# Optimization experiments

Measured on AMD Instinct MI355X. Metric: run time of the kernel, lower is better.

## Reference

```python
import jax, jax.numpy as jnp
import numpy as np

EPS = 1e-5   # torch F.layer_norm default eps
TOP_K = 20   # int(3*D^2 / (2*hr*N^2 + 10*D)) for D=768, N=196, hr=1.0
NUM_EXPERTS = 200  # 10 * TOP_K


def setup_inputs() -> dict:
    key = jax.random.key(0)
    ks = jax.random.split(key, 6)
    B, N, D = 32, 196, 768
    E, H = NUM_EXPERTS, 196  # H = int(N * hidden_ratio)
    s = 0.02
    return {
        "x": jax.random.normal(ks[0], (B, N, D), jnp.float32),
        "Wr": jax.random.normal(ks[1], (E, D), jnp.float32) * s,   # router.weight
        "W1": jax.random.normal(ks[2], (E, H, N), jnp.float32) * s,  # fc1.weight per expert
        "b1": jnp.zeros((E, H), jnp.float32),
        "W2": jax.random.normal(ks[3], (E, N, H), jnp.float32) * s,  # fc2.weight per expert
        "b2": jnp.zeros((E, N), jnp.float32),
        "Wo": jax.random.normal(ks[4], (D, D), jnp.float32) * s,     # out_proj.weight
        "bo": jnp.zeros((D,), jnp.float32),
    }


def reference(x, Wr, W1, b1, W2, b2, Wo, bo):
    B, N, D = x.shape
    E = Wr.shape[0]
    K = TOP_K

    # Router: per-sample routing on token-mean features
    logits = x.mean(axis=1) @ Wr.T                      # (B, E)
    probs = jax.nn.softmax(logits, axis=-1)             # (B, E)
    w, idx = jax.lax.top_k(probs, K)                    # (B, K) sorted desc, as torch.topk
    w = w / w.sum(axis=-1, keepdims=True)               # renormalize top-k weights

    # TokenMixer operates in (B, D, N) space: layernorm over tokens (no affine),
    # then fc1 (N->H), gelu(tanh), fc2 (H->N).
    xt = jnp.swapaxes(x, 1, 2)                          # (B, D, N)
    mu = xt.mean(axis=-1, keepdims=True)
    var = xt.var(axis=-1, keepdims=True)                # population var (matches F.layer_norm)
    z = (xt - mu) * jax.lax.rsqrt(var + EPS)            # (B, D, N)

    # Gather each sample's K expert weight matrices and batch the MLPs.
    W1g, b1g = W1[idx], b1[idx]                         # (B,K,H,N), (B,K,H)
    W2g, b2g = W2[idx], b2[idx]                         # (B,K,N,H), (B,K,N)

    h = jnp.einsum('bdn,bkhn->bkdh', z, W1g) + b1g[:, :, None, :]
    a = jax.nn.gelu(h, approximate=True)                # tanh-approx GELU
    o = jnp.einsum('bkdh,bknh->bkdn', a, W2g) + b2g[:, :, None, :]

    # Weighted combine over the K selected experts, back to (B, N, D)
    mix = jnp.einsum('bk,bkdn->bnd', w, o)

    out = mix @ Wo.T + bo                               # out_proj

    # Load-balancing aux loss (top-1 assignment fraction vs mean router prob)
    top1 = jax.nn.one_hot(idx[:, 0], E, dtype=probs.dtype)   # (B, E)
    aux = E * jnp.sum(probs.mean(axis=0) * top1.mean(axis=0))
    return out, aux
```

## Files before the change

### kernel.cpp

```cpp
#include <hip/hip_runtime.h>
#include <math.h>

constexpr int B  = 32;
constexpr int N  = 196;
constexpr int D  = 768;
constexpr int E  = 200;
constexpr int TK = 20;

constexpr int NGRP = 4;
constexpr int PRB  = 14336;
constexpr int EXB  = 114688;
constexpr int LK   = 40;

typedef __bf16 bf16x8 __attribute__((ext_vector_type(8)));
typedef __bf16 bf16x4 __attribute__((ext_vector_type(4)));
typedef float  f32x4  __attribute__((ext_vector_type(4)));
typedef long   longx2 __attribute__((ext_vector_type(2)));
typedef unsigned char uchar;

#define GLDS16(gp, lp)                                                        \
  __builtin_amdgcn_global_load_lds(                                           \
      (const __attribute__((address_space(1))) void*)(gp),                    \
      (__attribute__((address_space(3))) void*)(lp), 16, 0, 0)

#define WAITVM12  __builtin_amdgcn_s_waitcnt(0x0F7C)
#define WAITVM8   __builtin_amdgcn_s_waitcnt(0x0F78)
#define WAITVM0   __builtin_amdgcn_s_waitcnt(0x0F70)
#define WAITLGKM0 __builtin_amdgcn_s_waitcnt(0xC07F)
#define BAR       __builtin_amdgcn_s_barrier()

__device__ __forceinline__ float gelu_fast(float x) {
  float u = x * fmaf(x * x, 0.044715f, 1.0f);
  float e = exp2f(-2.3022084f * u);
  return x * __builtin_amdgcn_rcpf(1.0f + e);
}

__device__ __forceinline__ uchar f32_to_f8(float v) {
  return (uchar)(__builtin_amdgcn_cvt_pk_fp8_f32(v, v, 0, false) & 0xff);
}

__global__ __launch_bounds__(256) void k_ln(const float* __restrict__ x,
                                            uchar* __restrict__ zb,
                                            float* __restrict__ mu) {
  int b = blockIdx.x / 12, dt = blockIdx.x % 12;
  int d0 = dt * 64;
  int t = threadIdx.x;
  int q = t >> 6, d = t & 63;
  __shared__ float ps[256], pq[256];
  __shared__ float ms[64], rss[64];
  __shared__ alignas(16) uchar zt[64 * 256];

  for (int i = t; i < 1024; i += 256) ((uint4*)zt)[i] = (uint4){0, 0, 0, 0};

  const float* xp = x + ((size_t)b * N + q * 49) * D + d0 + d;
  float v[49];
  float s = 0.f, sq = 0.f;
  #pragma unroll
  for (int n = 0; n < 49; ++n) {
    v[n] = xp[(size_t)n * D];
    s += v[n]; sq += v[n] * v[n];
  }
  ps[t] = s; pq[t] = sq;
  __syncthreads();
  if (t < 64) {
    float S = ps[t] + ps[t + 64] + ps[t + 128] + ps[t + 192];
    float Q = pq[t] + pq[t + 64] + pq[t + 128] + pq[t + 192];
    float m = S * (1.0f / N);
    float var = Q * (1.0f / N) - m * m;
    ms[t] = m; rss[t] = rsqrtf(var + 1e-5f);
    mu[(size_t)b * D + d0 + t] = m;
  }
  __syncthreads();
  float m = ms[d], r = rss[d];
  int dsw = (d >> 1) & 3;
  #pragma unroll
  for (int n = 0; n < 49; ++n) {
    int tok = q * 49 + n;
    int qp = ((tok >> 3) & 3) ^ dsw;
    int off = d * 256 + (tok >> 6) * 64 + qp * 16 + ((tok >> 5) & 1) * 8 + (tok & 7);
    zt[off] = f32_to_f8((v[n] - m) * r);
  }
  __syncthreads();
  #pragma unroll
  for (int pair = 0; pair < 4; ++pair) {
    uint4* dst = (uint4*)(zb + (((size_t)b * 4 + pair) * 768 + d0) * 64);
    dst[t] = ((const uint4*)zt)[(t >> 2) * 16 + pair * 4 + (t & 3)];
  }
}

__global__ __launch_bounds__(256) void k_prep(
    const float* __restrict__ W1, const float* __restrict__ W2,
    const float* __restrict__ Wo,
    uchar* __restrict__ Wf, __bf16* __restrict__ Wob,
    const float* __restrict__ mu, const float* __restrict__ Wr,
    float* __restrict__ probs, int* __restrict__ idxg,
    float* __restrict__ wg) {
  int bx = blockIdx.x;
  int t = threadIdx.x;
  __shared__ alignas(16) uchar ls[224 * 256];
  __shared__ float sp[E];
  __shared__ float smax, ssum;
  __shared__ float svals[TK];
  __shared__ int   sidx[TK];

  if (bx >= 976) {
    int b = bx - 976;
    int lane = t & 63, wave = t >> 6;
    float* smu = (float*)ls;
    for (int i = t; i < 768; i += 256) smu[i] = mu[(size_t)b * D + i];
    __syncthreads();
    const float4* m4 = (const float4*)smu;
    #pragma unroll 1
    for (int i = 0; i < 50; ++i) {
      int e = wave * 50 + i;
      const float4* wr4 = (const float4*)(Wr + (size_t)e * D);
      float acc = 0.f;
      #pragma unroll
      for (int j = 0; j < 3; ++j) {
        float4 w = wr4[lane + j * 64], mm = m4[lane + j * 64];
        acc = fmaf(w.x, mm.x, acc); acc = fmaf(w.y, mm.y, acc);
        acc = fmaf(w.z, mm.z, acc); acc = fmaf(w.w, mm.w, acc);
      }
      #pragma unroll
      for (int off = 32; off > 0; off >>= 1) acc += __shfl_down(acc, off);
      if (lane == 0) sp[e] = acc;
    }
    __syncthreads();
    if (t < 64) {
      float mx = -1e30f;
      for (int e = t; e < E; e += 64) mx = fmaxf(mx, sp[e]);
      #pragma unroll
      for (int off = 32; off > 0; off >>= 1) mx = fmaxf(mx, __shfl_down(mx, off));
      if (t == 0) smax = mx;
    }
    __syncthreads();
    if (t < E) sp[t] = exp2f((sp[t] - smax) * 1.44269504f);
    __syncthreads();
    if (t < 64) {
      float s = 0.f;
      for (int e = t; e < E; e += 64) s += sp[e];
      #pragma unroll
      for (int off = 32; off > 0; off >>= 1) s += __shfl_down(s, off);
      if (t == 0) ssum = s;
    }
    __syncthreads();
    if (t < E) {
      sp[t] = sp[t] / ssum;
      probs[(size_t)b * E + t] = sp[t];
    }
    __syncthreads();
    for (int k = 0; k < TK; ++k) {
      if (t < 64) {
        float bv = -1e30f; int bi = 0;
        for (int e = t; e < E; e += 64) {
          float v = sp[e];
          if (v > bv) { bv = v; bi = e; }
        }
        #pragma unroll
        for (int off = 32; off > 0; off >>= 1) {
          float ov = __shfl_down(bv, off);
          int   oi = __shfl_down(bi, off);
          if (ov > bv || (ov == bv && oi < bi)) { bv = ov; bi = oi; }
        }
        if (t == 0) {
          svals[k] = bv; sidx[k] = bi;
          sp[bi] = -2e30f;
        }
      }
      __syncthreads();
    }
    if (t == 0) {
      float s = 0.f;
      for (int k = 0; k < TK; ++k) s += svals[k];
      float inv = 1.0f / s;
      for (int k = 0; k < TK; ++k) {
        wg[b * TK + k]   = svals[k] * inv;
        idxg[b * TK + k] = sidx[k];
      }
    }
    return;
  }

  if (bx >= 400) {
    int i = (bx - 400) * 256 + t;
    float4 v = *(const float4*)&Wo[(size_t)i * 4];
    bf16x4 o = {(__bf16)v.x, (__bf16)v.y, (__bf16)v.z, (__bf16)v.w};
    *(bf16x4*)&Wob[(size_t)i * 4] = o;
    return;
  }
  int e = bx >> 1, mat = bx & 1;
  for (int i = t; i < 3584; i += 256) ((uint4*)ls)[i] = (uint4){0, 0, 0, 0};
  __syncthreads();
  const float* src = (mat ? W2 : W1) + (size_t)e * 196 * 196;
  for (int i = t; i < 196 * 49; i += 256) {
    int r = i / 49, c4 = (i - r * 49) * 4;
    float4 v = *(const float4*)&src[(size_t)r * 196 + c4];
    int lo = __builtin_amdgcn_cvt_pk_fp8_f32(v.x, v.y, 0, false);
    unsigned int pk = (unsigned int)__builtin_amdgcn_cvt_pk_fp8_f32(v.z, v.w, lo, true);
    *(unsigned int*)&ls[r * 256 + c4] = pk;
  }
  __syncthreads();
  uchar* dst = Wf + (size_t)e * EXB + mat * 4 * PRB;
  for (int s = t; s < 3584; s += 256) {
    int p = s / 896, rem = s - p * 896;
    int col = rem >> 2, qp = rem & 3;
    int ql = qp ^ ((col >> 1) & 3);
    unsigned long lo = *(const unsigned long*)&ls[col * 256 + p * 64 + ql * 8];
    unsigned long hi = *(const unsigned long*)&ls[col * 256 + p * 64 + 32 + ql * 8];
    longx2 o; o[0] = (long)lo; o[1] = (long)hi;
    *(longx2*)&dst[(size_t)s * 16] = o;
  }
}

__global__ __launch_bounds__(256, 2) void k_expert(
    const uchar* __restrict__ zb, const uchar* __restrict__ Wf,
    const float* __restrict__ b1, const float* __restrict__ b2,
    const int* __restrict__ idxg, const float* __restrict__ wg,
    __bf16* __restrict__ mixg) {
  __shared__ alignas(16) uchar pool[75776];
  __shared__ alignas(16) __bf16 b1s[5 * 196];
  __shared__ alignas(16) __bf16 b2s[5 * 196];
  __shared__ int   eidx_s[5];
  __shared__ float w_s[5];
  uchar* zs  = pool;
  uchar* at  = pool + 16384;
  uchar* wsb = pool + 32768;
  __bf16* tb = (__bf16*)pool;

  int xw = blockIdx.x & 7, rr_ = blockIdx.x >> 3;
  int j = rr_ / 12, dt = rr_ - j * 12;
  int gid = j * 8 + xw;
  int g = gid & 3, b = gid >> 2;
  int d0 = dt * 64;

  int t = threadIdx.x;
  int lane = t & 63, wave = t >> 6;
  int quad = lane >> 4, l16 = lane & 15;
  int wrow = (wave & 1) * 32;
  int wcol = (wave >> 1) * 112;
  int qp = quad ^ ((l16 >> 1) & 3);

  if (t < 5) {
    eidx_s[t] = idxg[b * TK + g * 5 + t];
    w_s[t]    = wg[b * TK + g * 5 + t];
  }
  for (int i = t; i < 980; i += 256) {
    int kk = i / 196, col = i - kk * 196;
    int ee = idxg[b * TK + g * 5 + kk];
    b1s[i] = (__bf16)b1[ee * 196 + col];
    b2s[i] = (__bf16)b2[ee * 196 + col];
  }
  *(unsigned long*)&at[3 * 4096 + (t >> 2) * 64 + (t & 3) * 16 + 8] = 0ul;
  __syncthreads();

  {
    const uchar* zbase = zb + ((size_t)b * 4 * 768 + d0) * 64;
    #pragma unroll
    for (int p = 0; p < 4; ++p)
      GLDS16(zbase + (size_t)p * (768 * 64) + t * 16, zs + p * 4096 + t * 16);
  }

  int s0 = t * 16, s1 = (t + 256) * 16, s2 = (t + 512) * 16;
  int s3 = ((t & 127) + 768) * 16;

  auto issue = [&](int qn) {
    int qq = qn > 39 ? 39 : qn;
    int kk2 = qq >> 3, rem = qq & 7;
    const uchar* src = Wf + (size_t)eidx_s[kk2] * EXB + rem * PRB;
    int bi = qn & 3;
    uchar* lb = (bi == 3) ? pool : wsb + bi * PRB;
    GLDS16(src + s0, lb + s0);
    GLDS16(src + s1, lb + s1);
    GLDS16(src + s2, lb + s2);
    GLDS16(src + s3, lb + s3);
  };
  issue(0); issue(1); issue(2);

  WAITVM12;
  BAR;
  longx2 zf[4][2];
  #pragma unroll
  for (int p = 0; p < 4; ++p) {
    zf[p][0] = *(const longx2*)&zs[p * 4096 + (wrow + l16) * 64 + qp * 16];
    zf[p][1] = *(const longx2*)&zs[p * 4096 + (wrow + 16 + l16) * 64 + qp * 16];
  }

  f32x4 macc[14];
  #pragma unroll
  for (int i = 0; i < 14; ++i) macc[i] = (f32x4){0.f, 0.f, 0.f, 0.f};

  #pragma unroll 1
  for (int kk = 0; kk < 5; ++kk) {
    float wkv = w_s[kk];
    f32x4 hacc[14];
    #pragma unroll
    for (int i = 0; i < 14; ++i) hacc[i] = (f32x4){0.f, 0.f, 0.f, 0.f};

    #pragma unroll 1
    for (int p = 0; p < 4; ++p) {
      int q = kk * 8 + p;
      WAITVM8;
      BAR;
      int bi = q & 3;
      const uchar* buf = (bi == 3) ? pool : wsb + bi * PRB;
      __builtin_amdgcn_s_setprio(1);
      #pragma unroll
      for (int ct = 0; ct < 7; ++ct) {
        longx2 bf = *(const longx2*)&buf[(wcol + ct * 16 + l16) * 64 + qp * 16];
        hacc[ct]     = __builtin_amdgcn_mfma_f32_16x16x32_fp8_fp8(bf[0], zf[p][0][0], hacc[ct], 0, 0, 0);
        hacc[ct]     = __builtin_amdgcn_mfma_f32_16x16x32_fp8_fp8(bf[1], zf[p][0][1], hacc[ct], 0, 0, 0);
        hacc[7 + ct] = __builtin_amdgcn_mfma_f32_16x16x32_fp8_fp8(bf[0], zf[p][1][0], hacc[7 + ct], 0, 0, 0);
        hacc[7 + ct] = __builtin_amdgcn_mfma_f32_16x16x32_fp8_fp8(bf[1], zf[p][1][1], hacc[7 + ct], 0, 0, 0);
      }
      __builtin_amdgcn_s_setprio(0);
      issue(q + 3);
    }

    #pragma unroll
    for (int ct = 0; ct < 7; ++ct) {
      int hb = wcol + ct * 16 + quad * 4;
      bool valid = hb < 196;
      unsigned pk0 = 0u, pk1 = 0u;
      if (valid) {
        bf16x4 b4 = *(const bf16x4*)&b1s[kk * 196 + hb];
        float bv0 = (float)b4[0], bv1 = (float)b4[1];
        float bv2 = (float)b4[2], bv3 = (float)b4[3];
        f32x4 h0 = hacc[ct], h1 = hacc[7 + ct];
        pk0 = (unsigned)__builtin_amdgcn_cvt_pk_fp8_f32(
                  gelu_fast(h0[0] + bv0) * wkv, gelu_fast(h0[1] + bv1) * wkv, 0, false);
        pk0 = (unsigned)__builtin_amdgcn_cvt_pk_fp8_f32(
                  gelu_fast(h0[2] + bv2) * wkv, gelu_fast(h0[3] + bv3) * wkv, (int)pk0, true);
        pk1 = (unsigned)__builtin_amdgcn_cvt_pk_fp8_f32(
                  gelu_fast(h1[0] + bv0) * wkv, gelu_fast(h1[1] + bv1) * wkv, 0, false);
        pk1 = (unsigned)__builtin_amdgcn_cvt_pk_fp8_f32(
                  gelu_fast(h1[2] + bv2) * wkv, gelu_fast(h1[3] + bv3) * wkv, (int)pk1, true);
      }
      int d0r = wrow + l16;
      int addr0 = (hb >> 6) * 4096 + d0r * 64 + ((((hb >> 3) & 3) ^ ((d0r >> 1) & 3)) << 4)
                + ((hb >> 5) & 1) * 8 + (quad & 1) * 4;
      *(unsigned*)&at[addr0]        = pk0;
      *(unsigned*)&at[addr0 + 1024] = pk1;
    }
    WAITLGKM0;

    #pragma unroll 1
    for (int p = 0; p < 4; ++p) {
      int q = kk * 8 + 4 + p;
      WAITVM8;
      BAR;
      int bi = q & 3;
      const uchar* buf = (bi == 3) ? pool : wsb + bi * PRB;
      longx2 a0 = *(const longx2*)&at[p * 4096 + (wrow + l16) * 64 + qp * 16];
      longx2 a1 = *(const longx2*)&at[p * 4096 + (wrow + 16 + l16) * 64 + qp * 16];
      __builtin_amdgcn_s_setprio(1);
      #pragma unroll
      for (int ct = 0; ct < 7; ++ct) {
        longx2 bf = *(const longx2*)&buf[(wcol + ct * 16 + l16) * 64 + qp * 16];
        macc[ct]     = __builtin_amdgcn_mfma_f32_16x16x32_fp8_fp8(a0[0], bf[0], macc[ct], 0, 0, 0);
        macc[ct]     = __builtin_amdgcn_mfma_f32_16x16x32_fp8_fp8(a0[1], bf[1], macc[ct], 0, 0, 0);
        macc[7 + ct] = __builtin_amdgcn_mfma_f32_16x16x32_fp8_fp8(a1[0], bf[0], macc[7 + ct], 0, 0, 0);
        macc[7 + ct] = __builtin_amdgcn_mfma_f32_16x16x32_fp8_fp8(a1[1], bf[1], macc[7 + ct], 0, 0, 0);
      }
      __builtin_amdgcn_s_setprio(0);
      issue(q + 3);
    }
  }

  WAITVM0;
  BAR;
  #pragma unroll
  for (int ct = 0; ct < 7; ++ct) {
    int ncol = wcol + ct * 16 + l16;
    float bsum = 0.f;
    if (ncol < 196) {
      #pragma unroll
      for (int k5 = 0; k5 < 5; ++k5)
        bsum += w_s[k5] * (float)b2s[k5 * 196 + ncol];
    }
    #pragma unroll
    for (int rt = 0; rt < 2; ++rt) {
      f32x4 v = macc[rt * 7 + ct];
      bf16x4 o = {(__bf16)(v[0] + bsum), (__bf16)(v[1] + bsum),
                  (__bf16)(v[2] + bsum), (__bf16)(v[3] + bsum)};
      *(bf16x4*)&tb[ncol * 68 + wrow + rt * 16 + quad * 4] = o;
    }
  }
  __syncthreads();
  __bf16* mp = mixg + ((size_t)(g * B + b) * N) * D + d0;
  #pragma unroll
  for (int i = 0; i < 7; ++i) {
    int s = i * 256 + t;
    if (s < 1568) {
      int n = s >> 3, c = s & 7;
      const uint2* pa = (const uint2*)&tb[n * 68 + c * 8];
      uint2 v0 = pa[0], v1 = pa[1];
      uint4 v = {v0.x, v0.y, v1.x, v1.y};
      *(uint4*)&mp[(size_t)n * D + c * 8] = v;
    }
  }
}

__global__ __launch_bounds__(256, 2) void k_outproj(
    const __bf16* __restrict__ mixg, const __bf16* __restrict__ Wob,
    const float* __restrict__ bo, const float* __restrict__ probs,
    const int* __restrict__ idxg, float* __restrict__ out,
    float* __restrict__ out_aux) {
  __shared__ alignas(16) __bf16 As[32 * LK];
  __shared__ alignas(16) __bf16 Bs[256 * LK];
  const size_t GS = (size_t)B * N * D;

  int t = threadIdx.x;
  if (blockIdx.x == 0 && t < 32) {
    int top1 = idxg[t * TK];
    float s = 0.f;
    for (int bb = 0; bb < B; ++bb) s += probs[(size_t)bb * E + top1];
    #pragma unroll
    for (int off = 16; off > 0; off >>= 1) s += __shfl_down(s, off);
    if (t == 0) out_aux[0] = s * ((float)E / ((float)B * (float)B));
  }

  int m0 = (blockIdx.x % 196) * 32;
  int e0 = (blockIdx.x / 196) * 256;
  int lane = t & 63, wave = t >> 6;
  int quad = lane >> 4, l16 = lane & 15;
  int wrow = (wave & 1) * 16;
  int wcol = (wave >> 1) * 128;
  int arow = t >> 2, ach = t & 3;
  const __bf16* ap0 = mixg + (size_t)(m0 + (arow & 31)) * D + ach * 8;

  f32x4 acc[8];
  #pragma unroll
  for (int i = 0; i < 8; ++i) acc[i] = (f32x4){0.f, 0.f, 0.f, 0.f};

  const uint4* wsrc = (const uint4*)Wob;
  #pragma unroll 1
  for (int c = 0; c < 24; ++c) {
    int k0 = c * 32;
    __syncthreads();
    if (t < 128) {
      const __bf16* ap = ap0 + k0;
      bf16x8 g0 = *(const bf16x8*)(ap);
      bf16x8 g1 = *(const bf16x8*)(ap + GS);
      bf16x8 g2 = *(const bf16x8*)(ap + 2 * GS);
      bf16x8 g3 = *(const bf16x8*)(ap + 3 * GS);
      bf16x8 r;
      #pragma unroll
      for (int jj = 0; jj < 8; ++jj)
        r[jj] = (__bf16)((float)g0[jj] + (float)g1[jj] + (float)g2[jj] + (float)g3[jj]);
      *(bf16x8*)&As[arow * LK + ach * 8] = r;
    }
    for (int p = t; p < 1024; p += 256) {
      int rr = p >> 2, sub = p & 3;
      uint4 v = wsrc[(((size_t)(e0 + rr)) * D + k0) / 8 + sub];
      *(uint4*)&Bs[rr * LK + sub * 8] = v;
    }
    __syncthreads();
    bf16x8 a0 = *(const bf16x8*)&As[(wrow + l16) * LK + quad * 8];
    #pragma unroll
    for (int ct = 0; ct < 8; ++ct) {
      bf16x8 bfr = *(const bf16x8*)&Bs[(wcol + ct * 16 + l16) * LK + quad * 8];
      acc[ct] = __builtin_amdgcn_mfma_f32_16x16x32_bf16(a0, bfr, acc[ct], 0, 0, 0);
    }
  }

  #pragma unroll
  for (int ct = 0; ct < 8; ++ct) {
    int e = e0 + wcol + ct * 16 + l16;
    float bov = bo[e];
    #pragma unroll
    for (int rx = 0; rx < 4; ++rx) {
      int m = m0 + wrow + quad * 4 + rx;
      out[(size_t)m * D + e] = acc[ct][rx] + bov;
    }
  }
}

extern "C" void kernel_launch(void* const* d_in, const int* in_sizes, int n_in,
                              void* d_out, int out_size, void* d_ws, size_t ws_size,
                              hipStream_t stream) {
  const float* x  = (const float*)d_in[0];
  const float* Wr = (const float*)d_in[1];
  const float* W1 = (const float*)d_in[2];
  const float* b1 = (const float*)d_in[3];
  const float* W2 = (const float*)d_in[4];
  const float* b2 = (const float*)d_in[5];
  const float* Wo = (const float*)d_in[6];
  const float* bo = (const float*)d_in[7];
  float* out = (float*)d_out;

  char* p = (char*)d_ws;
  auto alloc = [&](size_t bytes) {
    char* r = p;
    p += (bytes + 255) & ~(size_t)255;
    return r;
  };
  uchar*  zb   = (uchar*)alloc((size_t)B * 4 * 768 * 64);
  float*  mu   = (float*)alloc((size_t)B * D * 4);
  uchar*  Wf   = (uchar*)alloc((size_t)E * EXB);
  __bf16* Wob  = (__bf16*)alloc((size_t)D * D * 2);
  __bf16* mixg = (__bf16*)alloc((size_t)NGRP * B * N * D * 2);
  float*  probs= (float*)alloc((size_t)B * E * 4);
  int*    idxg = (int*)alloc((size_t)B * TK * 4);
  float*  wg   = (float*)alloc((size_t)B * TK * 4);

  k_ln<<<dim3(B * 12), dim3(256), 0, stream>>>(x, zb, mu);
  k_prep<<<dim3(1008), dim3(256), 0, stream>>>(W1, W2, Wo, Wf, Wob,
                                               mu, Wr, probs, idxg, wg);
  k_expert<<<dim3(1536), dim3(256), 0, stream>>>(zb, Wf, b1, b2, idxg, wg, mixg);
  k_outproj<<<dim3(588), dim3(256), 0, stream>>>(mixg, Wob, bo, probs, idxg,
                                                 out, out + (size_t)B * N * D);
}
```

Before: 358.5 us.

## Merge layernorm into prep kernel and shrink expert LDS for higher occupancy

Folds the layernorm kernel into the prep kernel, with the router now computing token means itself from x, which removes one launch and the mu buffer. The expert kernel goes from a 3-deep to a 2-deep weight pipeline and aliases the z staging into the activation buffer, so shared memory shrinks from about 76KB to about 45KB and launch bounds rise to 3 blocks per CU. Expert bias sums are precomputed once per block, and outproj launch bounds rise to 4. The costs are shallower prefetch, an extra barrier per stage, and a router block that rereads all of x.

```diff
diff --git a/kernel.cpp b/kernel.cpp
--- a/kernel.cpp
+++ b/kernel.cpp
@@ -23,8 +23,8 @@
       (const __attribute__((address_space(1))) void*)(gp),                    \
       (__attribute__((address_space(3))) void*)(lp), 16, 0, 0)
 
-#define WAITVM12  __builtin_amdgcn_s_waitcnt(0x0F7C)
 #define WAITVM8   __builtin_amdgcn_s_waitcnt(0x0F78)
+#define WAITVM4   __builtin_amdgcn_s_waitcnt(0x0F74)
 #define WAITVM0   __builtin_amdgcn_s_waitcnt(0x0F70)
 #define WAITLGKM0 __builtin_amdgcn_s_waitcnt(0xC07F)
 #define BAR       __builtin_amdgcn_s_barrier()
@@ -39,192 +39,201 @@
   return (uchar)(__builtin_amdgcn_cvt_pk_fp8_f32(v, v, 0, false) & 0xff);
 }
 
-__global__ __launch_bounds__(256) void k_ln(const float* __restrict__ x,
-                                            uchar* __restrict__ zb,
-                                            float* __restrict__ mu) {
-  int b = blockIdx.x / 12, dt = blockIdx.x % 12;
-  int d0 = dt * 64;
-  int t = threadIdx.x;
-  int q = t >> 6, d = t & 63;
-  __shared__ float ps[256], pq[256];
-  __shared__ float ms[64], rss[64];
-  __shared__ alignas(16) uchar zt[64 * 256];
-
-  for (int i = t; i < 1024; i += 256) ((uint4*)zt)[i] = (uint4){0, 0, 0, 0};
-
-  const float* xp = x + ((size_t)b * N + q * 49) * D + d0 + d;
-  float v[49];
-  float s = 0.f, sq = 0.f;
-  #pragma unroll
-  for (int n = 0; n < 49; ++n) {
-    v[n] = xp[(size_t)n * D];
-    s += v[n]; sq += v[n] * v[n];
-  }
-  ps[t] = s; pq[t] = sq;
-  __syncthreads();
-  if (t < 64) {
-    float S = ps[t] + ps[t + 64] + ps[t + 128] + ps[t + 192];
-    float Q = pq[t] + pq[t + 64] + pq[t + 128] + pq[t + 192];
-    float m = S * (1.0f / N);
-    float var = Q * (1.0f / N) - m * m;
-    ms[t] = m; rss[t] = rsqrtf(var + 1e-5f);
-    mu[(size_t)b * D + d0 + t] = m;
-  }
-  __syncthreads();
-  float m = ms[d], r = rss[d];
-  int dsw = (d >> 1) & 3;
-  #pragma unroll
-  for (int n = 0; n < 49; ++n) {
-    int tok = q * 49 + n;
-    int qp = ((tok >> 3) & 3) ^ dsw;
-    int off = d * 256 + (tok >> 6) * 64 + qp * 16 + ((tok >> 5) & 1) * 8 + (tok & 7);
-    zt[off] = f32_to_f8((v[n] - m) * r);
-  }
-  __syncthreads();
-  #pragma unroll
-  for (int pair = 0; pair < 4; ++pair) {
-    uint4* dst = (uint4*)(zb + (((size_t)b * 4 + pair) * 768 + d0) * 64);
-    dst[t] = ((const uint4*)zt)[(t >> 2) * 16 + pair * 4 + (t & 3)];
-  }
-}
-
 __global__ __launch_bounds__(256) void k_prep(
+    const float* __restrict__ x,
     const float* __restrict__ W1, const float* __restrict__ W2,
-    const float* __restrict__ Wo,
-    uchar* __restrict__ Wf, __bf16* __restrict__ Wob,
-    const float* __restrict__ mu, const float* __restrict__ Wr,
+    const float* __restrict__ Wo, const float* __restrict__ Wr,
+    uchar* __restrict__ zb, uchar* __restrict__ Wf, __bf16* __restrict__ Wob,
     float* __restrict__ probs, int* __restrict__ idxg,
     float* __restrict__ wg) {
   int bx = blockIdx.x;
   int t = threadIdx.x;
-  __shared__ alignas(16) uchar ls[224 * 256];
+  __shared__ alignas(16) uchar ls[57344];
   __shared__ float sp[E];
   __shared__ float smax, ssum;
   __shared__ float svals[TK];
   __shared__ int   sidx[TK];
 
-  if (bx >= 976) {
-    int b = bx - 976;
-    int lane = t & 63, wave = t >> 6;
-    float* smu = (float*)ls;
-    for (int i = t; i < 768; i += 256) smu[i] = mu[(size_t)b * D + i];
-    __syncthreads();
-    const float4* m4 = (const float4*)smu;
-    #pragma unroll 1
-    for (int i = 0; i < 50; ++i) {
-      int e = wave * 50 + i;
-      const float4* wr4 = (const float4*)(Wr + (size_t)e * D);
-      float acc = 0.f;
-      #pragma unroll
-      for (int j = 0; j < 3; ++j) {
-        float4 w = wr4[lane + j * 64], mm = m4[lane + j * 64];
-        acc = fmaf(w.x, mm.x, acc); acc = fmaf(w.y, mm.y, acc);
-        acc = fmaf(w.z, mm.z, acc); acc = fmaf(w.w, mm.w, acc);
-      }
-      #pragma unroll
-      for (int off = 32; off > 0; off >>= 1) acc += __shfl_down(acc, off);
-      if (lane == 0) sp[e] = acc;
-    }
+  if (bx < 384) {
+    int b = bx / 12, dt = bx % 12;
+    int d0 = dt * 64;
+    int q = t >> 6, d = t & 63;
+    uchar* zt = ls;
+    float* ps = (float*)(ls + 16384);
+    float* pq = ps + 256;
+    float* ms = pq + 256;
+    float* rss = ms + 64;
+
+    for (int i = t; i < 1024; i += 256) ((uint4*)zt)[i] = (uint4){0, 0, 0, 0};
+
+    const float* xp = x + ((size_t)b * N + q * 49) * D + d0 + d;
+    float v[49];
+    float s = 0.f, sq = 0.f;
+    #pragma unroll
+    for (int n = 0; n < 49; ++n) {
+      v[n] = xp[(size_t)n * D];
+      s += v[n]; sq += v[n] * v[n];
+    }
+    ps[t] = s; pq[t] = sq;
     __syncthreads();
     if (t < 64) {
-      float mx = -1e30f;
-      for (int e = t; e < E; e += 64) mx = fmaxf(mx, sp[e]);
-      #pragma unroll
-      for (int off = 32; off > 0; off >>= 1) mx = fmaxf(mx, __shfl_down(mx, off));
-      if (t == 0) smax = mx;
-    }
-    __syncthreads();
-    if (t < E) sp[t] = exp2f((sp[t] - smax) * 1.44269504f);
-    __syncthreads();
-    if (t < 64) {
-      float s = 0.f;
-      for (int e = t; e < E; e += 64) s += sp[e];
-      #pragma unroll
-      for (int off = 32; off > 0; off >>= 1) s += __shfl_down(s, off);
-      if (t == 0) ssum = s;
-    }
-    __syncthreads();
-    if (t < E) {
-      sp[t] = sp[t] / ssum;
-      probs[(size_t)b * E + t] = sp[t];
-    }
-    __syncthreads();
-    for (int k = 0; k < TK; ++k) {
-      if (t < 64) {
-        float bv = -1e30f; int bi = 0;
-        for (int e = t; e < E; e += 64) {
-          float v = sp[e];
-          if (v > bv) { bv = v; bi = e; }
-        }
-        #pragma unroll
-        for (int off = 32; off > 0; off >>= 1) {
-          float ov = __shfl_down(bv, off);
-          int   oi = __shfl_down(bi, off);
-          if (ov > bv || (ov == bv && oi < bi)) { bv = ov; bi = oi; }
-        }
-        if (t == 0) {
-          svals[k] = bv; sidx[k] = bi;
-          sp[bi] = -2e30f;
-        }
-      }
-      __syncthreads();
-    }
-    if (t == 0) {
-      float s = 0.f;
-      for (int k = 0; k < TK; ++k) s += svals[k];
-      float inv = 1.0f / s;
-      for (int k = 0; k < TK; ++k) {
-        wg[b * TK + k]   = svals[k] * inv;
-        idxg[b * TK + k] = sidx[k];
-      }
+      float S = ps[t] + ps[t + 64] + ps[t + 128] + ps[t + 192];
+      float Q = pq[t] + pq[t + 64] + pq[t + 128] + pq[t + 192];
+      float m = S * (1.0f / N);
+      float var = Q * (1.0f / N) - m * m;
+      ms[t] = m; rss[t] = rsqrtf(var + 1e-5f);
+    }
+    __syncthreads();
+    float m = ms[d], r = rss[d];
+    int dsw = (d >> 1) & 3;
+    #pragma unroll
+    for (int n = 0; n < 49; ++n) {
+      int tok = q * 49 + n;
+      int qp = ((tok >> 3) & 3) ^ dsw;
+      int off = d * 256 + (tok >> 6) * 64 + qp * 16 + ((tok >> 5) & 1) * 8 + (tok & 7);
+      zt[off] = f32_to_f8((v[n] - m) * r);
+    }
+    __syncthreads();
+    #pragma unroll
+    for (int pair = 0; pair < 4; ++pair) {
+      uint4* dst = (uint4*)(zb + (((size_t)b * 4 + pair) * 768 + d0) * 64);
+      dst[t] = ((const uint4*)zt)[(t >> 2) * 16 + pair * 4 + (t & 3)];
     }
     return;
   }
 
-  if (bx >= 400) {
-    int i = (bx - 400) * 256 + t;
+  if (bx < 784) {
+    int e = (bx - 384) >> 1, mat = (bx - 384) & 1;
+    for (int i = t; i < 3584; i += 256) ((uint4*)ls)[i] = (uint4){0, 0, 0, 0};
+    __syncthreads();
+    const float* src = (mat ? W2 : W1) + (size_t)e * 196 * 196;
+    for (int i = t; i < 196 * 49; i += 256) {
+      int r = i / 49, c4 = (i - r * 49) * 4;
+      float4 v = *(const float4*)&src[(size_t)r * 196 + c4];
+      int lo = __builtin_amdgcn_cvt_pk_fp8_f32(v.x, v.y, 0, false);
+      unsigned int pk = (unsigned int)__builtin_amdgcn_cvt_pk_fp8_f32(v.z, v.w, lo, true);
+      *(unsigned int*)&ls[r * 256 + c4] = pk;
+    }
+    __syncthreads();
+    uchar* dst = Wf + (size_t)e * EXB + mat * 4 * PRB;
+    for (int s = t; s < 3584; s += 256) {
+      int p = s / 896, rem = s - p * 896;
+      int col = rem >> 2, qp = rem & 3;
+      int ql = qp ^ ((col >> 1) & 3);
+      unsigned long lo = *(const unsigned long*)&ls[col * 256 + p * 64 + ql * 8];
+      unsigned long hi = *(const unsigned long*)&ls[col * 256 + p * 64 + 32 + ql * 8];
+      longx2 o; o[0] = (long)lo; o[1] = (long)hi;
+      *(longx2*)&dst[(size_t)s * 16] = o;
+    }
+    return;
+  }
+
+  if (bx < 1360) {
+    int i = (bx - 784) * 256 + t;
     float4 v = *(const float4*)&Wo[(size_t)i * 4];
     bf16x4 o = {(__bf16)v.x, (__bf16)v.y, (__bf16)v.z, (__bf16)v.w};
     *(bf16x4*)&Wob[(size_t)i * 4] = o;
     return;
   }
-  int e = bx >> 1, mat = bx & 1;
-  for (int i = t; i < 3584; i += 256) ((uint4*)ls)[i] = (uint4){0, 0, 0, 0};
-  __syncthreads();
-  const float* src = (mat ? W2 : W1) + (size_t)e * 196 * 196;
-  for (int i = t; i < 196 * 49; i += 256) {
-    int r = i / 49, c4 = (i - r * 49) * 4;
-    float4 v = *(const float4*)&src[(size_t)r * 196 + c4];
-    int lo = __builtin_amdgcn_cvt_pk_fp8_f32(v.x, v.y, 0, false);
-    unsigned int pk = (unsigned int)__builtin_amdgcn_cvt_pk_fp8_f32(v.z, v.w, lo, true);
-    *(unsigned int*)&ls[r * 256 + c4] = pk;
-  }
-  __syncthreads();
-  uchar* dst = Wf + (size_t)e * EXB + mat * 4 * PRB;
-  for (int s = t; s < 3584; s += 256) {
-    int p = s / 896, rem = s - p * 896;
-    int col = rem >> 2, qp = rem & 3;
-    int ql = qp ^ ((col >> 1) & 3);
-    unsigned long lo = *(const unsigned long*)&ls[col * 256 + p * 64 + ql * 8];
-    unsigned long hi = *(const unsigned long*)&ls[col * 256 + p * 64 + 32 + ql * 8];
-    longx2 o; o[0] = (long)lo; o[1] = (long)hi;
-    *(longx2*)&dst[(size_t)s * 16] = o;
+
+  int b = bx - 1360;
+  int lane = t & 63, wave = t >> 6;
+  float* smu = (float*)ls;
+  {
+    const float* xb = x + (size_t)b * N * D;
+    float a0 = 0.f, a1 = 0.f, a2 = 0.f;
+    #pragma unroll 4
+    for (int n = 0; n < 196; ++n) {
+      const float* rp = xb + (size_t)n * D + t;
+      a0 += rp[0]; a1 += rp[256]; a2 += rp[512];
+    }
+    const float inv = 1.0f / (float)N;
+    smu[t] = a0 * inv; smu[t + 256] = a1 * inv; smu[t + 512] = a2 * inv;
+  }
+  __syncthreads();
+  const float4* m4 = (const float4*)smu;
+  #pragma unroll 1
+  for (int i = 0; i < 50; ++i) {
+    int e = wave * 50 + i;
+    const float4* wr4 = (const float4*)(Wr + (size_t)e * D);
+    float acc = 0.f;
+    #pragma unroll
+    for (int j = 0; j < 3; ++j) {
+      float4 w = wr4[lane + j * 64], mm = m4[lane + j * 64];
+      acc = fmaf(w.x, mm.x, acc); acc = fmaf(w.y, mm.y, acc);
+      acc = fmaf(w.z, mm.z, acc); acc = fmaf(w.w, mm.w, acc);
+    }
+    #pragma unroll
+    for (int off = 32; off > 0; off >>= 1) acc += __shfl_down(acc, off);
+    if (lane == 0) sp[e] = acc;
+  }
+  __syncthreads();
+  if (t < 64) {
+    float mx = -1e30f;
+    for (int e = t; e < E; e += 64) mx = fmaxf(mx, sp[e]);
+    #pragma unroll
+    for (int off = 32; off > 0; off >>= 1) mx = fmaxf(mx, __shfl_down(mx, off));
+    if (t == 0) smax = mx;
+  }
+  __syncthreads();
+  if (t < E) sp[t] = exp2f((sp[t] - smax) * 1.44269504f);
+  __syncthreads();
+  if (t < 64) {
+    float s = 0.f;
+    for (int e = t; e < E; e += 64) s += sp[e];
+    #pragma unroll
+    for (int off = 32; off > 0; off >>= 1) s += __shfl_down(s, off);
+    if (t == 0) ssum = s;
+  }
+  __syncthreads();
+  if (t < E) {
+    sp[t] = sp[t] / ssum;
+    probs[(size_t)b * E + t] = sp[t];
+  }
+  __syncthreads();
+  for (int k = 0; k < TK; ++k) {
+    if (t < 64) {
+      float bv = -1e30f; int bi = 0;
+      for (int e = t; e < E; e += 64) {
+        float v = sp[e];
+        if (v > bv) { bv = v; bi = e; }
+      }
+      #pragma unroll
+      for (int off = 32; off > 0; off >>= 1) {
+        float ov = __shfl_down(bv, off);
+        int   oi = __shfl_down(bi, off);
+        if (ov > bv || (ov == bv && oi < bi)) { bv = ov; bi = oi; }
+      }
+      if (t == 0) {
+        svals[k] = bv; sidx[k] = bi;
+        sp[bi] = -2e30f;
+      }
+    }
+    __syncthreads();
+  }
+  if (t == 0) {
+    float s = 0.f;
+    for (int k = 0; k < TK; ++k) s += svals[k];
+    float inv = 1.0f / s;
+    for (int k = 0; k < TK; ++k) {
+      wg[b * TK + k]   = svals[k] * inv;
+      idxg[b * TK + k] = sidx[k];
+    }
   }
 }
 
-__global__ __launch_bounds__(256, 2) void k_expert(
+__global__ __launch_bounds__(256, 3) void k_expert(
     const uchar* __restrict__ zb, const uchar* __restrict__ Wf,
     const float* __restrict__ b1, const float* __restrict__ b2,
     const int* __restrict__ idxg, const float* __restrict__ wg,
     __bf16* __restrict__ mixg) {
-  __shared__ alignas(16) uchar pool[75776];
+  __shared__ alignas(16) uchar pool[45056];
   __shared__ alignas(16) __bf16 b1s[5 * 196];
-  __shared__ alignas(16) __bf16 b2s[5 * 196];
+  __shared__ float bsum_s[196];
   __shared__ int   eidx_s[5];
   __shared__ float w_s[5];
-  uchar* zs  = pool;
-  uchar* at  = pool + 16384;
-  uchar* wsb = pool + 32768;
+  uchar* wsb = pool;
+  uchar* at  = pool + 28672;
   __bf16* tb = (__bf16*)pool;
 
   int xw = blockIdx.x & 7, rr_ = blockIdx.x >> 3;
@@ -248,42 +257,53 @@
     int kk = i / 196, col = i - kk * 196;
     int ee = idxg[b * TK + g * 5 + kk];
     b1s[i] = (__bf16)b1[ee * 196 + col];
-    b2s[i] = (__bf16)b2[ee * 196 + col];
-  }
-  *(unsigned long*)&at[3 * 4096 + (t >> 2) * 64 + (t & 3) * 16 + 8] = 0ul;
+  }
+  if (t < 196) {
+    float s = 0.f;
+    #pragma unroll
+    for (int k5 = 0; k5 < 5; ++k5) {
+      int ee = idxg[b * TK + g * 5 + k5];
+      s += wg[b * TK + g * 5 + k5] * b2[ee * 196 + t];
+    }
+    bsum_s[t] = s;
+  }
   __syncthreads();
 
   {
     const uchar* zbase = zb + ((size_t)b * 4 * 768 + d0) * 64;
     #pragma unroll
     for (int p = 0; p < 4; ++p)
-      GLDS16(zbase + (size_t)p * (768 * 64) + t * 16, zs + p * 4096 + t * 16);
+      GLDS16(zbase + (size_t)p * (768 * 64) + t * 16, at + p * 4096 + t * 16);
   }
 
   int s0 = t * 16, s1 = (t + 256) * 16, s2 = (t + 512) * 16;
   int s3 = ((t & 127) + 768) * 16;
-
   auto issue = [&](int qn) {
     int qq = qn > 39 ? 39 : qn;
     int kk2 = qq >> 3, rem = qq & 7;
     const uchar* src = Wf + (size_t)eidx_s[kk2] * EXB + rem * PRB;
-    int bi = qn & 3;
-    uchar* lb = (bi == 3) ? pool : wsb + bi * PRB;
+    uchar* lb = wsb + (qn & 1) * PRB;
     GLDS16(src + s0, lb + s0);
     GLDS16(src + s1, lb + s1);
     GLDS16(src + s2, lb + s2);
     GLDS16(src + s3, lb + s3);
   };
-  issue(0); issue(1); issue(2);
-
-  WAITVM12;
+  issue(0); issue(1);
+
+  WAITVM8;
   BAR;
+  const uchar* abase = at + (wrow + l16) * 64 + qp * 16;
   longx2 zf[4][2];
   #pragma unroll
   for (int p = 0; p < 4; ++p) {
-    zf[p][0] = *(const longx2*)&zs[p * 4096 + (wrow + l16) * 64 + qp * 16];
-    zf[p][1] = *(const longx2*)&zs[p * 4096 + (wrow + 16 + l16) * 64 + qp * 16];
-  }
+    zf[p][0] = *(const longx2*)(abase + p * 4096);
+    zf[p][1] = *(const longx2*)(abase + p * 4096 + 1024);
+  }
+  WAITLGKM0;
+  BAR;
+  *(unsigned long*)&at[3 * 4096 + (t >> 2) * 64 + (t & 3) * 16 + 8] = 0ul;
+
+  const uchar* bbase0 = wsb + (wcol + l16) * 64 + qp * 16;
 
   f32x4 macc[14];
   #pragma unroll
@@ -299,21 +319,22 @@
     #pragma unroll 1
     for (int p = 0; p < 4; ++p) {
       int q = kk * 8 + p;
-      WAITVM8;
+      WAITVM4;
       BAR;
-      int bi = q & 3;
-      const uchar* buf = (bi == 3) ? pool : wsb + bi * PRB;
+      const uchar* bb = bbase0 + (q & 1) * PRB;
       __builtin_amdgcn_s_setprio(1);
       #pragma unroll
       for (int ct = 0; ct < 7; ++ct) {
-        longx2 bf = *(const longx2*)&buf[(wcol + ct * 16 + l16) * 64 + qp * 16];
+        longx2 bf = *(const longx2*)(bb + ct * 1024);
         hacc[ct]     = __builtin_amdgcn_mfma_f32_16x16x32_fp8_fp8(bf[0], zf[p][0][0], hacc[ct], 0, 0, 0);
         hacc[ct]     = __builtin_amdgcn_mfma_f32_16x16x32_fp8_fp8(bf[1], zf[p][0][1], hacc[ct], 0, 0, 0);
         hacc[7 + ct] = __builtin_amdgcn_mfma_f32_16x16x32_fp8_fp8(bf[0], zf[p][1][0], hacc[7 + ct], 0, 0, 0);
         hacc[7 + ct] = __builtin_amdgcn_mfma_f32_16x16x32_fp8_fp8(bf[1], zf[p][1][1], hacc[7 + ct], 0, 0, 0);
       }
       __builtin_amdgcn_s_setprio(0);
-      issue(q + 3);
+      WAITLGKM0;
+      BAR;
+      issue(q + 2);
     }
 
     #pragma unroll
@@ -346,23 +367,24 @@
     #pragma unroll 1
     for (int p = 0; p < 4; ++p) {
       int q = kk * 8 + 4 + p;
-      WAITVM8;
+      WAITVM4;
       BAR;
-      int bi = q & 3;
-      const uchar* buf = (bi == 3) ? pool : wsb + bi * PRB;
-      longx2 a0 = *(const longx2*)&at[p * 4096 + (wrow + l16) * 64 + qp * 16];
-      longx2 a1 = *(const longx2*)&at[p * 4096 + (wrow + 16 + l16) * 64 + qp * 16];
+      const uchar* bb = bbase0 + (q & 1) * PRB;
+      longx2 a0 = *(const longx2*)(abase + p * 4096);
+      longx2 a1 = *(const longx2*)(abase + p * 4096 + 1024);
       __builtin_amdgcn_s_setprio(1);
       #pragma unroll
       for (int ct = 0; ct < 7; ++ct) {
-        longx2 bf = *(const longx2*)&buf[(wcol + ct * 16 + l16) * 64 + qp * 16];
+        longx2 bf = *(const longx2*)(bb + ct * 1024);
         macc[ct]     = __builtin_amdgcn_mfma_f32_16x16x32_fp8_fp8(a0[0], bf[0], macc[ct], 0, 0, 0);
         macc[ct]     = __builtin_amdgcn_mfma_f32_16x16x32_fp8_fp8(a0[1], bf[1], macc[ct], 0, 0, 0);
         macc[7 + ct] = __builtin_amdgcn_mfma_f32_16x16x32_fp8_fp8(a1[0], bf[0], macc[7 + ct], 0, 0, 0);
         macc[7 + ct] = __builtin_amdgcn_mfma_f32_16x16x32_fp8_fp8(a1[1], bf[1], macc[7 + ct], 0, 0, 0);
       }
       __builtin_amdgcn_s_setprio(0);
-      issue(q + 3);
+      WAITLGKM0;
+      BAR;
+      issue(q + 2);
     }
   }
 
@@ -371,12 +393,7 @@
   #pragma unroll
   for (int ct = 0; ct < 7; ++ct) {
     int ncol = wcol + ct * 16 + l16;
-    float bsum = 0.f;
-    if (ncol < 196) {
-      #pragma unroll
-      for (int k5 = 0; k5 < 5; ++k5)
-        bsum += w_s[k5] * (float)b2s[k5 * 196 + ncol];
-    }
+    float bsum = (ncol < 196) ? bsum_s[ncol] : 0.f;
     #pragma unroll
     for (int rt = 0; rt < 2; ++rt) {
       f32x4 v = macc[rt * 7 + ct];
@@ -400,7 +417,7 @@
   }
 }
 
-__global__ __launch_bounds__(256, 2) void k_outproj(
+__global__ __launch_bounds__(256, 4) void k_outproj(
     const __bf16* __restrict__ mixg, const __bf16* __restrict__ Wob,
     const float* __restrict__ bo, const float* __restrict__ probs,
     const int* __restrict__ idxg, float* __restrict__ out,
@@ -495,7 +512,6 @@
     return r;
   };
   uchar*  zb   = (uchar*)alloc((size_t)B * 4 * 768 * 64);
-  float*  mu   = (float*)alloc((size_t)B * D * 4);
   uchar*  Wf   = (uchar*)alloc((size_t)E * EXB);
   __bf16* Wob  = (__bf16*)alloc((size_t)D * D * 2);
   __bf16* mixg = (__bf16*)alloc((size_t)NGRP * B * N * D * 2);
@@ -503,9 +519,8 @@
   int*    idxg = (int*)alloc((size_t)B * TK * 4);
   float*  wg   = (float*)alloc((size_t)B * TK * 4);
 
-  k_ln<<<dim3(B * 12), dim3(256), 0, stream>>>(x, zb, mu);
-  k_prep<<<dim3(1008), dim3(256), 0, stream>>>(W1, W2, Wo, Wf, Wob,
-                                               mu, Wr, probs, idxg, wg);
+  k_prep<<<dim3(1392), dim3(256), 0, stream>>>(x, W1, W2, Wo, Wr,
+                                               zb, Wf, Wob, probs, idxg, wg);
   k_expert<<<dim3(1536), dim3(256), 0, stream>>>(zb, Wf, b1, b2, idxg, wg, mixg);
   k_outproj<<<dim3(588), dim3(256), 0, stream>>>(mixg, Wob, bo, probs, idxg,
                                                  out, out + (size_t)B * N * D);
```

Measured after the change: 371.5 us. 1.04x slower.
